# Optimization experiments

Measured on AMD Instinct MI355X. Metric: run time of the kernel, lower is better.

The kernel has to match this reference:

```python
import jax, jax.numpy as jnp
import numpy as np

N = 50000
E = 800000
IN_DIM = 128
HID = 32
HEADS = 2
OUT_DIM = 32
EPS = 1e-5          # BatchNorm eps
SLOPE = 0.2         # LeakyReLU negative slope (PyG GATConv default)


def gat_conv(x, src, dst, W, a_src, a_dst, bias, heads, out_dim, concat):
    """PyG-style GATConv (self-loops already appended to src/dst)."""
    n = x.shape[0]
    h = (x @ W).reshape(n, heads, out_dim)            # [N, H, D]
    # per-node attention contributions  [N, H]
    e_src = jnp.sum(h * a_src, axis=-1)
    e_dst = jnp.sum(h * a_dst, axis=-1)
    # per-edge logits [Etot, H]
    e = jax.nn.leaky_relu(e_src[src] + e_dst[dst], SLOPE)
    # segment softmax over destination node
    emax = jax.ops.segment_max(e, dst, num_segments=n)
    emax = jnp.where(jnp.isfinite(emax), emax, 0.0)
    ex = jnp.exp(e - emax[dst])
    denom = jax.ops.segment_sum(ex, dst, num_segments=n)
    alpha = ex / (denom[dst] + 1e-16)                 # [Etot, H]
    # weighted message aggregation
    out = jax.ops.segment_sum(alpha[:, :, None] * h[src], dst, num_segments=n)
    out = out.reshape(n, heads * out_dim) if concat else out.mean(axis=1)
    return out + bias


def batch_norm(x, gamma, beta):
    # training-mode BatchNorm1d over the node (batch) dimension, biased var
    mu = x.mean(axis=0)
    var = x.var(axis=0)
    return (x - mu) * jax.lax.rsqrt(var + EPS) * gamma + beta


def setup_inputs() -> dict:
    key = jax.random.key(0)
    ks = jax.random.split(key, 12)
    s = 0.1
    return {
        "x": jax.random.normal(ks[0], (N, IN_DIM), jnp.float32),
        "W1": jax.random.normal(ks[1], (IN_DIM, HEADS * HID), jnp.float32) * s,
        "as1": jax.random.normal(ks[2], (HEADS, HID), jnp.float32) * s,
        "ad1": jax.random.normal(ks[3], (HEADS, HID), jnp.float32) * s,
        "b1": jnp.zeros((HEADS * HID,), jnp.float32),
        "g1": jnp.ones((HEADS * HID,), jnp.float32),
        "be1": jnp.zeros((HEADS * HID,), jnp.float32),
        "W2": jax.random.normal(ks[4], (HEADS * HID, HEADS * HID), jnp.float32) * s,
        "as2": jax.random.normal(ks[5], (HEADS, HID), jnp.float32) * s,
        "ad2": jax.random.normal(ks[6], (HEADS, HID), jnp.float32) * s,
        "b2": jnp.zeros((HEADS * HID,), jnp.float32),
        "g2": jnp.ones((HEADS * HID,), jnp.float32),
        "be2": jnp.zeros((HEADS * HID,), jnp.float32),
        "W3": jax.random.normal(ks[7], (HEADS * HID, OUT_DIM), jnp.float32) * s,
        "as3": jax.random.normal(ks[8], (1, OUT_DIM), jnp.float32) * s,
        "ad3": jax.random.normal(ks[9], (1, OUT_DIM), jnp.float32) * s,
        "b3": jnp.zeros((OUT_DIM,), jnp.float32),
        "g3": jnp.ones((OUT_DIM,), jnp.float32),
        "be3": jnp.zeros((OUT_DIM,), jnp.float32),
        "edge_index": jax.random.randint(ks[10], (2, E), 0, N, jnp.int64 if jax.config.jax_enable_x64 else jnp.int32),
    }


def reference(x, W1, as1, ad1, b1, g1, be1,
              W2, as2, ad2, b2, g2, be2,
              W3, as3, ad3, b3, g3, be3, edge_index):
    n = x.shape[0]
    loops = jnp.arange(n, dtype=edge_index.dtype)
    src = jnp.concatenate([edge_index[0], loops])  # add_self_loops=True
    dst = jnp.concatenate([edge_index[1], loops])
    h = gat_conv(x, src, dst, W1, as1, ad1, b1, HEADS, HID, True)
    h = jax.nn.relu(batch_norm(h, g1, be1))
    h = gat_conv(h, src, dst, W2, as2, ad2, b2, HEADS, HID, True)
    h = jax.nn.relu(batch_norm(h, g2, be2))
    h = gat_conv(h, src, dst, W3, as3, ad3, b3, 1, OUT_DIM, False)
    h = jax.nn.relu(batch_norm(h, g3, be3))
    return h
```

## Files before the change

### kernel.cpp

```cpp
#include <hip/hip_runtime.h>


__device__ __forceinline__ float lrelu(float x) { return x > 0.f ? x : 0.2f * x; }
__device__ __forceinline__ unsigned short f2bf(float x) {
    unsigned u = __float_as_uint(x);
    return (unsigned short)((u + 0x7FFFu + ((u >> 16) & 1u)) >> 16);
}
__device__ __forceinline__ float bf2f(unsigned short v) {
    return __uint_as_float(((unsigned)v) << 16);
}

template <int K, int OUTF, int H, bool FUSE>
__device__ __forceinline__ void gemm_attn_body(
    int vbid, const float* __restrict__ in, const float* __restrict__ W,
    const float* __restrict__ scale, const float* __restrict__ shift,
    const float* __restrict__ a_src, const float* __restrict__ a_dst,
    unsigned short* __restrict__ hb, float* __restrict__ es,
    float* __restrict__ ed, int N)
{
    constexpr int BK = 32;
    constexpr int M = 128;
    constexpr int XS = BK + 4;
    constexpr int HS = OUTF / 32;
    constexpr int NC = K / BK;
    __shared__ float xs[M * XS];
    __shared__ float wsl[32 * XS];
    __shared__ float redS[8 * 132];
    __shared__ float redD[8 * 132];

    const int tid = threadIdx.x;
    const int tile = (HS == 2) ? (vbid >> 1) : vbid;
    const int hs = (HS == 2) ? (vbid & 1) : 0;
    const int n0 = tile * M;
    const int jb = hs * 32;

    const int lane = tid & 31;
    const int jt = (tid >> 5) * 4;
    const int kq4 = (tid & 7) * 4;
    const int nrow = tid >> 3;
    const int wj = tid & 31;
    const int wk = tid >> 5;

    float acc[4][4];
#pragma unroll
    for (int i = 0; i < 4; ++i)
#pragma unroll
        for (int jj = 0; jj < 4; ++jj) acc[i][jj] = 0.f;

    float4 xr[4];
    float wr[4];

#pragma unroll
    for (int i = 0; i < 4; ++i) {
        int gn = n0 + nrow + 32 * i;
        if (gn >= N) gn = N - 1;
        xr[i] = *(const float4*)(in + (size_t)gn * K + kq4);
    }
#pragma unroll
    for (int i = 0; i < 4; ++i)
        wr[i] = W[(size_t)(wk + 8 * i) * OUTF + jb + wj];

#pragma unroll 1
    for (int c = 0; c < NC; ++c) {
        const int kc = c * BK;
        float4 sc, sh;
        if constexpr (FUSE) {
            sc = *(const float4*)(scale + kc + kq4);
            sh = *(const float4*)(shift + kc + kq4);
        }
        __syncthreads();
#pragma unroll
        for (int i = 0; i < 4; ++i) {
            float4 v = xr[i];
            if constexpr (FUSE) {
                v.x = fmaxf(v.x * sc.x + sh.x, 0.f);
                v.y = fmaxf(v.y * sc.y + sh.y, 0.f);
                v.z = fmaxf(v.z * sc.z + sh.z, 0.f);
                v.w = fmaxf(v.w * sc.w + sh.w, 0.f);
            }
            *(float4*)&xs[(nrow + 32 * i) * XS + kq4] = v;
        }
#pragma unroll
        for (int i = 0; i < 4; ++i)
            wsl[wj * XS + wk + 8 * i] = wr[i];
        __syncthreads();
        if (c + 1 < NC) {
            const int kn = kc + BK;
#pragma unroll
            for (int i = 0; i < 4; ++i) {
                int gn = n0 + nrow + 32 * i;
                if (gn >= N) gn = N - 1;
                xr[i] = *(const float4*)(in + (size_t)gn * K + kn + kq4);
            }
#pragma unroll
            for (int i = 0; i < 4; ++i)
                wr[i] = W[(size_t)(kn + wk + 8 * i) * OUTF + jb + wj];
        }
#pragma unroll
        for (int k4 = 0; k4 < BK; k4 += 4) {
            float4 xv[4];
#pragma unroll
            for (int i = 0; i < 4; ++i)
                xv[i] = *(float4*)&xs[(lane + 32 * i) * XS + k4];
#pragma unroll
            for (int jj = 0; jj < 4; ++jj) {
                float4 wv = *(float4*)&wsl[(jt + jj) * XS + k4];
#pragma unroll
                for (int i = 0; i < 4; ++i)
                    acc[i][jj] += xv[i].x * wv.x + xv[i].y * wv.y
                                + xv[i].z * wv.z + xv[i].w * wv.w;
            }
        }
    }

    const int jg = tid >> 5;
#pragma unroll
    for (int i = 0; i < 4; ++i) {
        int r = lane + 32 * i;
        int gn = n0 + r;
        float p = 0.f, q = 0.f;
#pragma unroll
        for (int jj = 0; jj < 4; ++jj) {
            p += acc[i][jj] * a_src[jb + jt + jj];
            q += acc[i][jj] * a_dst[jb + jt + jj];
        }
        if (gn < N) {
            uint2 u;
            u.x = (unsigned)f2bf(acc[i][0]) | ((unsigned)f2bf(acc[i][1]) << 16);
            u.y = (unsigned)f2bf(acc[i][2]) | ((unsigned)f2bf(acc[i][3]) << 16);
            *(uint2*)(hb + (size_t)gn * OUTF + jb + jt) = u;
        }
        redS[jg * 132 + r] = p;
        redD[jg * 132 + r] = q;
    }
    __syncthreads();
    if (tid < M) {
        int gn = n0 + tid;
        if (gn < N) {
            float e = 0.f, d = 0.f;
#pragma unroll
            for (int g = 0; g < 8; ++g) {
                e += redS[g * 132 + tid];
                d += redD[g * 132 + tid];
            }
            es[gn * H + hs] = e;
            ed[gn * H + hs] = d;
        }
    }
}

template <int K, int OUTF, int H, bool FUSE>
__global__ __launch_bounds__(256) void gemm_attn_k(
    const float* __restrict__ in, const float* __restrict__ W,
    const float* __restrict__ scale, const float* __restrict__ shift,
    const float* __restrict__ a_src, const float* __restrict__ a_dst,
    unsigned short* __restrict__ hb, float* __restrict__ es,
    float* __restrict__ ed, int N)
{
    gemm_attn_body<K, OUTF, H, FUSE>(blockIdx.x, in, W, scale, shift,
                                     a_src, a_dst, hb, es, ed, N);
}

template <int K, int OUTF, int H>
__global__ __launch_bounds__(256) void gemm_scatter_k(
    const int* __restrict__ ei, int* __restrict__ cur,
    unsigned short* __restrict__ colE, int E, int GB,
    const float* __restrict__ in, const float* __restrict__ W,
    const float* __restrict__ a_src, const float* __restrict__ a_dst,
    unsigned short* __restrict__ hb, float* __restrict__ es,
    float* __restrict__ ed, int N)
{
    if (blockIdx.x >= GB) {
        int e0 = (blockIdx.x - GB) * 2048 + threadIdx.x * 8;
        if (e0 + 8 <= E) {
            int4 sa = *(const int4*)(ei + e0);
            int4 sb = *(const int4*)(ei + e0 + 4);
            int4 da = *(const int4*)(ei + E + e0);
            int4 db = *(const int4*)(ei + E + e0 + 4);
            int ss[8] = {sa.x, sa.y, sa.z, sa.w, sb.x, sb.y, sb.z, sb.w};
            int dd[8] = {da.x, da.y, da.z, da.w, db.x, db.y, db.z, db.w};
            int pos[8];
#pragma unroll
            for (int u = 0; u < 8; ++u)
                pos[u] = atomicAdd(&cur[dd[u]], 1) & 63;
#pragma unroll
            for (int u = 0; u < 8; ++u)
                colE[((size_t)dd[u] << 6) + pos[u]] = (unsigned short)ss[u];
        } else {
            int i = e0 - E;
            if (i >= 0) {
#pragma unroll
                for (int u = 0; u < 8; ++u) {
                    int d = i + u;
                    if (d < N) {
                        int pos = atomicAdd(&cur[d], 1) & 63;
                        colE[((size_t)d << 6) + pos] = (unsigned short)d;
                    }
                }
            }
        }
        return;
    }
    gemm_attn_body<K, OUTF, H, false>(blockIdx.x, in, W, nullptr, nullptr,
                                      a_src, a_dst, hb, es, ed, N);
}

template <int H>
__global__ __launch_bounds__(256) void node_sg_k(
    const int* __restrict__ degA, const unsigned short* __restrict__ colE,
    const float* __restrict__ es, const float* __restrict__ ed,
    const unsigned short* __restrict__ hb, float* __restrict__ out,
    float* __restrict__ psum, float* __restrict__ psumsq, int N)
{
    constexpr int LPN = H * 16;
    constexpr int F = LPN * 2;
    constexpr int NPB = 256 / LPN;
    int t = blockIdx.x * 256 + threadIdx.x;
    int node = t / LPN;
    int lane = t - node * LPN;
    const bool valid = node < N;

    const uint* h2 = (const uint*)hb;
    const float2* es2 = (const float2*)es;

    size_t base = (size_t)node << 6;
    int deg = 0;
    float ed0 = 0.f, ed1 = 0.f;
    if (valid) {
        deg = degA[node];
        if (deg > 64) deg = 64;
        if constexpr (H == 2) {
            float2 e = ((const float2*)ed)[node];
            ed0 = e.x; ed1 = e.y;
        } else {
            ed0 = ed[node];
        }
    }

    int sc_ = 0;
    float x0 = 0.f, x1 = 0.f;
    if (lane < deg) {
        sc_ = colE[base + lane];
        if constexpr (H == 2) {
            float2 v = es2[sc_];
            x0 = __expf(lrelu(v.x + ed0));
            x1 = __expf(lrelu(v.y + ed1));
        } else {
            x0 = __expf(lrelu(es[sc_] + ed0));
        }
    }
    float s0 = x0, s1 = x1;
    for (int e = lane + LPN; e < deg; e += LPN) {
        int s = colE[base + e];
        if constexpr (H == 2) {
            float2 v = es2[s];
            s0 += __expf(lrelu(v.x + ed0));
            s1 += __expf(lrelu(v.y + ed1));
        } else {
            s0 += __expf(lrelu(es[s] + ed0));
        }
    }

    const int dcap = deg < LPN ? deg : LPN;
    const bool pre = (dcap >= 8);
    int sI0[8];
    uint v0[8];
    if (pre) {
#pragma unroll
        for (int u = 0; u < 8; ++u) sI0[u] = __shfl(sc_, u, LPN);
#pragma unroll
        for (int u = 0; u < 8; ++u) v0[u] = h2[(size_t)sI0[u] * LPN + lane];
    }

#pragma unroll
    for (int m = LPN / 2; m; m >>= 1) {
        s0 += __shfl_xor(s0, m, LPN);
        if (H == 2) s1 += __shfl_xor(s1, m, LPN);
    }
    float rd0 = 1.f / (s0 + 1e-16f);
    float rd1 = (H == 2) ? 1.f / (s1 + 1e-16f) : 0.f;

    const bool hi = (H == 2) && (lane >= 16);
    float acc0 = 0.f, acc1 = 0.f;
    int e = 0;
    if (pre) {
        float a[8];
#pragma unroll
        for (int u = 0; u < 8; ++u) {
            float a0 = __shfl(x0, u, LPN);
            if constexpr (H == 2) {
                float a1 = __shfl(x1, u, LPN);
                a[u] = hi ? a1 * rd1 : a0 * rd0;
            } else {
                a[u] = a0 * rd0;
            }
        }
#pragma unroll
        for (int u = 0; u < 8; ++u) {
            acc0 += a[u] * bf2f((unsigned short)v0[u]);
            acc1 += a[u] * bf2f((unsigned short)(v0[u] >> 16));
        }
        e = 8;
    }
    for (; e + 8 <= dcap; e += 8) {
        int sI[8];
        float a[8];
#pragma unroll
        for (int u = 0; u < 8; ++u) {
            sI[u] = __shfl(sc_, e + u, LPN);
            float a0 = __shfl(x0, e + u, LPN);
            if constexpr (H == 2) {
                float a1 = __shfl(x1, e + u, LPN);
                a[u] = hi ? a1 * rd1 : a0 * rd0;
            } else {
                a[u] = a0 * rd0;
            }
        }
        uint v[8];
#pragma unroll
        for (int u = 0; u < 8; ++u) v[u] = h2[(size_t)sI[u] * LPN + lane];
#pragma unroll
        for (int u = 0; u < 8; ++u) {
            acc0 += a[u] * bf2f((unsigned short)v[u]);
            acc1 += a[u] * bf2f((unsigned short)(v[u] >> 16));
        }
    }
    for (; e + 4 <= dcap; e += 4) {
        int sI[4];
        float a[4];
#pragma unroll
        for (int u = 0; u < 4; ++u) {
            sI[u] = __shfl(sc_, e + u, LPN);
            float a0 = __shfl(x0, e + u, LPN);
            if constexpr (H == 2) {
                float a1 = __shfl(x1, e + u, LPN);
                a[u] = hi ? a1 * rd1 : a0 * rd0;
            } else {
                a[u] = a0 * rd0;
            }
        }
        uint v[4];
#pragma unroll
        for (int u = 0; u < 4; ++u) v[u] = h2[(size_t)sI[u] * LPN + lane];
#pragma unroll
        for (int u = 0; u < 4; ++u) {
            acc0 += a[u] * bf2f((unsigned short)v[u]);
            acc1 += a[u] * bf2f((unsigned short)(v[u] >> 16));
        }
    }
    for (; e < dcap; ++e) {
        int sI = __shfl(sc_, e, LPN);
        float a0 = __shfl(x0, e, LPN);
        float a;
        if constexpr (H == 2) {
            float a1 = __shfl(x1, e, LPN);
            a = hi ? a1 * rd1 : a0 * rd0;
        } else {
            a = a0 * rd0;
        }
        uint v = h2[(size_t)sI * LPN + lane];
        acc0 += a * bf2f((unsigned short)v);
        acc1 += a * bf2f((unsigned short)(v >> 16));
    }
    for (int e2 = LPN; e2 < deg; ++e2) {
        int s = colE[base + e2];
        float a;
        if constexpr (H == 2) {
            float2 vv = es2[s];
            a = hi ? __expf(lrelu(vv.y + ed1)) * rd1
                   : __expf(lrelu(vv.x + ed0)) * rd0;
        } else {
            a = __expf(lrelu(es[s] + ed0)) * rd0;
        }
        uint v = h2[(size_t)s * LPN + lane];
        acc0 += a * bf2f((unsigned short)v);
        acc1 += a * bf2f((unsigned short)(v >> 16));
    }
    if (valid)
        ((float2*)out)[(size_t)node * LPN + lane] = make_float2(acc0, acc1);

    __shared__ float ls0[256], ls1[256];
    ls0[threadIdx.x] = acc0;
    ls1[threadIdx.x] = acc1;
    __syncthreads();
    if (threadIdx.x < LPN) {
        int l = threadIdx.x;
        float t0 = 0.f, t0q = 0.f, t1 = 0.f, t1q = 0.f;
#pragma unroll
        for (int g = 0; g < NPB; ++g) {
            float v0_ = ls0[g * LPN + l], v1_ = ls1[g * LPN + l];
            t0 += v0_; t0q += v0_ * v0_;
            t1 += v1_; t1q += v1_ * v1_;
        }
        int slot = (blockIdx.x & 127) * F;
        atomicAdd(&psum[slot + 2 * l], t0);
        atomicAdd(&psum[slot + 2 * l + 1], t1);
        atomicAdd(&psumsq[slot + 2 * l], t0q);
        atomicAdd(&psumsq[slot + 2 * l + 1], t1q);
    }
}

__global__ void bn_final_k(float* __restrict__ psum,
                           float* __restrict__ psumsq,
                           const float* __restrict__ gamma,
                           const float* __restrict__ beta,
                           float* __restrict__ scale, float* __restrict__ shift,
                           int N, int F)
{
    int f = threadIdx.x % F;
    int r = threadIdx.x / F;
    int R = 256 / F;
    float s = 0.f, s2 = 0.f;
    for (int b = r; b < 128; b += R) {
        s += psum[b * F + f];
        s2 += psumsq[b * F + f];
        psum[b * F + f] = 0.f;
        psumsq[b * F + f] = 0.f;
    }
    __shared__ float l1[256], l2[256];
    l1[threadIdx.x] = s;
    l2[threadIdx.x] = s2;
    __syncthreads();
    if (r == 0) {
        for (int g = 1; g < R; ++g) { s += l1[g * F + f]; s2 += l2[g * F + f]; }
        float inv = 1.f / (float)N;
        float mu = s * inv;
        float var = s2 * inv - mu * mu;
        var = fmaxf(var, 0.f);
        float rs = rsqrtf(var + 1e-5f);
        float sc = rs * gamma[f];
        scale[f] = sc;
        shift[f] = beta[f] - mu * sc;
    }
}

__global__ __launch_bounds__(256) void out_final_k(
    const float* __restrict__ x, const float* __restrict__ scale,
    const float* __restrict__ shift, float* __restrict__ out, int total)
{
    int i = blockIdx.x * 256 + threadIdx.x;
    if (i >= total) return;
    int f = i & 31;
    out[i] = fmaxf(x[i] * scale[f] + shift[f], 0.f);
}


extern "C" void kernel_launch(void* const* d_in, const int* in_sizes, int n_in,
                              void* d_out, int out_size, void* d_ws,
                              size_t ws_size, hipStream_t stream)
{
    const float* x   = (const float*)d_in[0];
    const float* W1  = (const float*)d_in[1];
    const float* as1 = (const float*)d_in[2];
    const float* ad1 = (const float*)d_in[3];
    const float* g1  = (const float*)d_in[5];
    const float* be1 = (const float*)d_in[6];
    const float* W2  = (const float*)d_in[7];
    const float* as2 = (const float*)d_in[8];
    const float* ad2 = (const float*)d_in[9];
    const float* g2  = (const float*)d_in[11];
    const float* be2 = (const float*)d_in[12];
    const float* W3  = (const float*)d_in[13];
    const float* as3 = (const float*)d_in[14];
    const float* ad3 = (const float*)d_in[15];
    const float* g3  = (const float*)d_in[17];
    const float* be3 = (const float*)d_in[18];
    const int*   ei  = (const int*)d_in[19];

    const int N  = in_sizes[0] / 128;
    const int E  = in_sizes[19] / 2;
    const int Et = E + N;

    float* ws = (float*)d_ws;
    size_t off = 0;
    unsigned short* Hb = (unsigned short*)(ws + off); off += (size_t)N * 32;
    float* AGG = ws + off;  off += (size_t)N * 64;
    float* ES  = ws + off;  off += (size_t)N * 2;
    float* ED  = ws + off;  off += (size_t)N * 2;
    float* SC  = ws + off;  off += 64;
    float* SH  = ws + off;  off += 64;
    size_t zOff = off;
    float* PS  = ws + off;  off += (size_t)128 * 64;
    float* PS2 = ws + off;  off += (size_t)128 * 64;
    int* cur   = (int*)(ws + off);  off += N;
    size_t zEnd = off;
    unsigned short* colE = (unsigned short*)(ws + off); off += (size_t)N * 32;

    const int tiles      = (N + 127) / 128;
    const int gemm2Blocks = tiles * 2;
    const int gemm1Blocks = tiles;
    const int sg64Blocks = (int)(((size_t)N * 32 + 255) / 256);
    const int sg32Blocks = (int)(((size_t)N * 16 + 255) / 256);
    const int edgeBlocks = (Et + 2047) / 2048;
    const int n32Blocks  = (N * 32 + 255) / 256;

    hipMemsetAsync(ws + zOff, 0, (zEnd - zOff) * sizeof(float), stream);
    gemm_scatter_k<128, 64, 2><<<gemm2Blocks + edgeBlocks, 256, 0, stream>>>(
        ei, cur, colE, E, gemm2Blocks,
        x, W1, as1, ad1, Hb, ES, ED, N);

    node_sg_k<2><<<sg64Blocks, 256, 0, stream>>>(cur, colE, ES, ED, Hb, AGG, PS, PS2, N);
    bn_final_k<<<1, 256, 0, stream>>>(PS, PS2, g1, be1, SC, SH, N, 64);

    gemm_attn_k<64, 64, 2, true><<<gemm2Blocks, 256, 0, stream>>>(
        AGG, W2, SC, SH, as2, ad2, Hb, ES, ED, N);
    node_sg_k<2><<<sg64Blocks, 256, 0, stream>>>(cur, colE, ES, ED, Hb, AGG, PS, PS2, N);
    bn_final_k<<<1, 256, 0, stream>>>(PS, PS2, g2, be2, SC, SH, N, 64);

    gemm_attn_k<64, 32, 1, true><<<gemm1Blocks, 256, 0, stream>>>(
        AGG, W3, SC, SH, as3, ad3, Hb, ES, ED, N);
    node_sg_k<1><<<sg32Blocks, 256, 0, stream>>>(cur, colE, ES, ED, Hb, AGG, PS, PS2, N);
    bn_final_k<<<1, 256, 0, stream>>>(PS, PS2, g3, be3, SC, SH, N, 32);
    out_final_k<<<n32Blocks, 256, 0, stream>>>(AGG, SC, SH, (float*)d_out, N * 32);
}
```

Baseline: 287.2 us.

## Halve GEMM row tile to 64 and drop register prefetch of next K-chunk

Shrinks the per-block node tile in the fused GEMM+attention kernel from 128 to 64 rows, which doubles the block count and cuts per-thread accumulators and shared memory. Each thread now loads 8 contiguous floats per row. The software prefetch of the next K chunk into registers is removed, so global loads are issued in the same iteration they are consumed. The goal is more parallelism and occupancy across the GPU, at the cost of exposed load latency and twice as many W reloads per node.

```diff
diff --git a/kernel.cpp b/kernel.cpp
--- a/kernel.cpp
+++ b/kernel.cpp
@@ -19,14 +19,14 @@
     float* __restrict__ ed, int N)
 {
     constexpr int BK = 32;
-    constexpr int M = 128;
+    constexpr int M = 64;
     constexpr int XS = BK + 4;
     constexpr int HS = OUTF / 32;
     constexpr int NC = K / BK;
     __shared__ float xs[M * XS];
     __shared__ float wsl[32 * XS];
-    __shared__ float redS[8 * 132];
-    __shared__ float redD[8 * 132];
+    __shared__ float redS[8 * 68];
+    __shared__ float redD[8 * 68];
 
     const int tid = threadIdx.x;
     const int tile = (HS == 2) ? (vbid >> 1) : vbid;
@@ -36,77 +36,65 @@
 
     const int lane = tid & 31;
     const int jt = (tid >> 5) * 4;
-    const int kq4 = (tid & 7) * 4;
-    const int nrow = tid >> 3;
+    const int kq8 = (tid & 3) * 8;
+    const int nrow = tid >> 2;
     const int wj = tid & 31;
     const int wk = tid >> 5;
 
-    float acc[4][4];
-#pragma unroll
-    for (int i = 0; i < 4; ++i)
+    float acc[2][4];
+#pragma unroll
+    for (int i = 0; i < 2; ++i)
 #pragma unroll
         for (int jj = 0; jj < 4; ++jj) acc[i][jj] = 0.f;
 
-    float4 xr[4];
-    float wr[4];
-
-#pragma unroll
-    for (int i = 0; i < 4; ++i) {
-        int gn = n0 + nrow + 32 * i;
-        if (gn >= N) gn = N - 1;
-        xr[i] = *(const float4*)(in + (size_t)gn * K + kq4);
-    }
-#pragma unroll
-    for (int i = 0; i < 4; ++i)
-        wr[i] = W[(size_t)(wk + 8 * i) * OUTF + jb + wj];
+    int gx = n0 + nrow;
+    if (gx >= N) gx = N - 1;
+    const float* xrow = in + (size_t)gx * K;
 
 #pragma unroll 1
     for (int c = 0; c < NC; ++c) {
         const int kc = c * BK;
-        float4 sc, sh;
+        float4 v0 = *(const float4*)(xrow + kc + kq8);
+        float4 v1 = *(const float4*)(xrow + kc + kq8 + 4);
         if constexpr (FUSE) {
-            sc = *(const float4*)(scale + kc + kq4);
-            sh = *(const float4*)(shift + kc + kq4);
-        }
+            float4 sc0 = *(const float4*)(scale + kc + kq8);
+            float4 sh0 = *(const float4*)(shift + kc + kq8);
+            float4 sc1 = *(const float4*)(scale + kc + kq8 + 4);
+            float4 sh1 = *(const float4*)(shift + kc + kq8 + 4);
+            v0.x = fmaxf(v0.x * sc0.x + sh0.x, 0.f);
+            v0.y = fmaxf(v0.y * sc0.y + sh0.y, 0.f);
+            v0.z = fmaxf(v0.z * sc0.z + sh0.z, 0.f);
+            v0.w = fmaxf(v0.w * sc0.w + sh0.w, 0.f);
+            v1.x = fmaxf(v1.x * sc1.x + sh1.x, 0.f);
+            v1.y = fmaxf(v1.y * sc1.y + sh1.y, 0.f);
+            v1.z = fmaxf(v1.z * sc1.z + sh1.z, 0.f);
+            v1.w = fmaxf(v1.w * sc1.w + sh1.w, 0.f);
+        }
+        float w0 = W[(size_t)(kc + wk) * OUTF + jb + wj];
+        float w1 = W[(size_t)(kc + wk + 8) * OUTF + jb + wj];
+        float w2 = W[(size_t)(kc + wk + 16) * OUTF + jb + wj];
+        float w3 = W[(size_t)(kc + wk + 24) * OUTF + jb + wj];
+
         __syncthreads();
-#pragma unroll
-        for (int i = 0; i < 4; ++i) {
-            float4 v = xr[i];
-            if constexpr (FUSE) {
-                v.x = fmaxf(v.x * sc.x + sh.x, 0.f);
-                v.y = fmaxf(v.y * sc.y + sh.y, 0.f);
-                v.z = fmaxf(v.z * sc.z + sh.z, 0.f);
-                v.w = fmaxf(v.w * sc.w + sh.w, 0.f);
-            }
-            *(float4*)&xs[(nrow + 32 * i) * XS + kq4] = v;
-        }
-#pragma unroll
-        for (int i = 0; i < 4; ++i)
-            wsl[wj * XS + wk + 8 * i] = wr[i];
+        *(float4*)&xs[nrow * XS + kq8] = v0;
+        *(float4*)&xs[nrow * XS + kq8 + 4] = v1;
+        wsl[wj * XS + wk] = w0;
+        wsl[wj * XS + wk + 8] = w1;
+        wsl[wj * XS + wk + 16] = w2;
+        wsl[wj * XS + wk + 24] = w3;
         __syncthreads();
-        if (c + 1 < NC) {
-            const int kn = kc + BK;
-#pragma unroll
-            for (int i = 0; i < 4; ++i) {
-                int gn = n0 + nrow + 32 * i;
-                if (gn >= N) gn = N - 1;
-                xr[i] = *(const float4*)(in + (size_t)gn * K + kn + kq4);
-            }
-#pragma unroll
-            for (int i = 0; i < 4; ++i)
-                wr[i] = W[(size_t)(kn + wk + 8 * i) * OUTF + jb + wj];
-        }
+
 #pragma unroll
         for (int k4 = 0; k4 < BK; k4 += 4) {
-            float4 xv[4];
-#pragma unroll
-            for (int i = 0; i < 4; ++i)
+            float4 xv[2];
+#pragma unroll
+            for (int i = 0; i < 2; ++i)
                 xv[i] = *(float4*)&xs[(lane + 32 * i) * XS + k4];
 #pragma unroll
             for (int jj = 0; jj < 4; ++jj) {
                 float4 wv = *(float4*)&wsl[(jt + jj) * XS + k4];
 #pragma unroll
-                for (int i = 0; i < 4; ++i)
+                for (int i = 0; i < 2; ++i)
                     acc[i][jj] += xv[i].x * wv.x + xv[i].y * wv.y
                                 + xv[i].z * wv.z + xv[i].w * wv.w;
             }
@@ -115,7 +103,7 @@
 
     const int jg = tid >> 5;
 #pragma unroll
-    for (int i = 0; i < 4; ++i) {
+    for (int i = 0; i < 2; ++i) {
         int r = lane + 32 * i;
         int gn = n0 + r;
         float p = 0.f, q = 0.f;
@@ -130,8 +118,8 @@
             u.y = (unsigned)f2bf(acc[i][2]) | ((unsigned)f2bf(acc[i][3]) << 16);
             *(uint2*)(hb + (size_t)gn * OUTF + jb + jt) = u;
         }
-        redS[jg * 132 + r] = p;
-        redD[jg * 132 + r] = q;
+        redS[jg * 68 + r] = p;
+        redD[jg * 68 + r] = q;
     }
     __syncthreads();
     if (tid < M) {
@@ -140,8 +128,8 @@
             float e = 0.f, d = 0.f;
 #pragma unroll
             for (int g = 0; g < 8; ++g) {
-                e += redS[g * 132 + tid];
-                d += redD[g * 132 + tid];
+                e += redS[g * 68 + tid];
+                d += redD[g * 68 + tid];
             }
             es[gn * H + hs] = e;
             ed[gn * H + hs] = d;
@@ -486,7 +474,7 @@
     size_t zEnd = off;
     unsigned short* colE = (unsigned short*)(ws + off); off += (size_t)N * 32;
 
-    const int tiles      = (N + 127) / 128;
+    const int tiles      = (N + 63) / 64;
     const int gemm2Blocks = tiles * 2;
     const int gemm1Blocks = tiles;
     const int sg64Blocks = (int)(((size_t)N * 32 + 255) / 256);
```

Result: no change. 285.5 us (median of 2 runs) (-0.6%).
